# Kernel tuning notes

Measured on AMD Instinct MI355X. Metric: run time of the kernel, lower is better.

The kernel has to match this reference:

```python
import jax, jax.numpy as jnp
import numpy as np

L, D, H, G, HS, I, V, B, T = 4, 1024, 16, 4, 64, 2816, 32000, 4, 512
THETA = 10000.0
EPS = 1e-6


def setup_inputs() -> dict:
    key = jax.random.key(0)
    ks = jax.random.split(key, 10)
    s = 0.02
    return {
        "input_ids": jax.random.randint(ks[0], (B, T), 0, V),
        "embed": jax.random.normal(ks[1], (V, D)) * s,      # tied with lm_head
        "q_w": jax.random.normal(ks[2], (L, D, D)) * s,     # torch Linear: [out, in]
        "q_b": jax.random.normal(ks[3], (L, D)) * s,
        "kv_w": jax.random.normal(ks[4], (L, 2 * G * HS, D)) * s,
        "kv_b": jax.random.normal(ks[5], (L, 2 * G * HS)) * s,
        "o_w": jax.random.normal(ks[6], (L, D, D)) * s,
        "ln1_w": jnp.ones((L, D)),
        "ln2_w": jnp.ones((L, D)),
        "gate_w": jax.random.normal(ks[7], (L, I, D)) * s,
        "up_w": jax.random.normal(ks[8], (L, I, D)) * s,
        "down_w": jax.random.normal(ks[9], (L, D, I)) * s,
        "last_w": jnp.ones((D,)),
    }


def rms_norm(x, w):
    return x * jax.lax.rsqrt(jnp.mean(x * x, axis=-1, keepdims=True) + EPS) * w


def rope_tables(t, hs):
    inv_freq = 1.0 / (THETA ** (jnp.arange(0, hs, 2, dtype=jnp.float32) / hs))
    ang = jnp.arange(t, dtype=jnp.float32)[:, None] * inv_freq[None, :]  # [T, hs/2]
    emb = jnp.concatenate([ang, ang], axis=-1)                           # [T, hs]
    return jnp.cos(emb), jnp.sin(emb)


def rotate_half(x):
    x1, x2 = jnp.split(x, 2, axis=-1)
    return jnp.concatenate([-x2, x1], axis=-1)


def reference(input_ids, embed, q_w, q_b, kv_w, kv_b, o_w, ln1_w, ln2_w, gate_w, up_w, down_w, last_w):
    x = embed[input_ids]  # [B, T, D]
    cos, sin = rope_tables(T, HS)                    # [T, HS] (buffers, const)
    c, s_ = cos[None, None], sin[None, None]         # [1, 1, T, HS]
    causal = jnp.tril(jnp.ones((T, T), dtype=bool))
    scale = 1.0 / np.sqrt(HS).astype(np.float32)
    for l in range(L):
        h = rms_norm(x, ln1_w[l])
        q = (h @ q_w[l].T + q_b[l]).reshape(B, T, H, HS).transpose(0, 2, 1, 3)  # bhtd
        kv = h @ kv_w[l].T + kv_b[l]
        k, v = jnp.split(kv, 2, axis=-1)
        k = k.reshape(B, T, G, HS).transpose(0, 2, 1, 3)  # bgtd
        v = v.reshape(B, T, G, HS).transpose(0, 2, 1, 3)
        k = jnp.repeat(k, H // G, axis=1)  # GQA kv repeat -> bhtd
        v = jnp.repeat(v, H // G, axis=1)
        q = q * c + rotate_half(q) * s_
        k = k * c + rotate_half(k) * s_
        attn = jnp.einsum('bhtd,bhsd->bhts', q, k) * scale
        attn = jnp.where(causal, attn, -jnp.inf)
        attn = jax.nn.softmax(attn, axis=-1)
        o = jnp.einsum('bhts,bhsd->bhtd', attn, v).transpose(0, 2, 1, 3).reshape(B, T, D)
        x = x + o @ o_w[l].T  # o_proj has no bias
        h = rms_norm(x, ln2_w[l])
        x = x + (jax.nn.silu(h @ gate_w[l].T) * (h @ up_w[l].T)) @ down_w[l].T  # SwiGLU
    x = rms_norm(x, last_w)
    return x @ embed.T  # tied lm_head -> logits [B, T, V]
```

## Files before the change

kernel.cpp:

```cpp
#include <hip/hip_runtime.h>
#include <hip/hip_bf16.h>
#include <stdint.h>


typedef __bf16 bf16x8 __attribute__((ext_vector_type(8)));
typedef __bf16 bf16x4 __attribute__((ext_vector_type(4)));
typedef float  f32x4  __attribute__((ext_vector_type(4)));

#define AS1 __attribute__((address_space(1)))
#define AS3 __attribute__((address_space(3)))

__device__ __forceinline__ void gld_lds16(const void* g, void* l) {
  __builtin_amdgcn_global_load_lds((const AS1 void*)g, (AS3 void*)l, 16, 0, 0);
}

__global__ __launch_bounds__(256) void cvt_kernel(const float* __restrict__ in,
                                                  __bf16* __restrict__ out, int n4) {
  for (int i = blockIdx.x * 256 + threadIdx.x; i < n4; i += gridDim.x * 256) {
    f32x4 v = ((const f32x4*)in)[i];
    bf16x4 o;
#pragma unroll
    for (int j = 0; j < 4; ++j) o[j] = (__bf16)v[j];
    ((bf16x4*)out)[i] = o;
  }
}

__global__ __launch_bounds__(256) void embed_kernel(const int* __restrict__ ids,
                                                    const float* __restrict__ emb,
                                                    float* __restrict__ x) {
  const int tok = blockIdx.x;
  const float* src = emb + (size_t)ids[tok] * 1024;
  float* dst = x + (size_t)tok * 1024;
#pragma unroll
  for (int j = 0; j < 4; ++j) {
    const int d = threadIdx.x + j * 256;
    dst[d] = src[d];
  }
}

__global__ __launch_bounds__(256) void rmsnorm_kernel(const float* __restrict__ x,
                                                      const float* __restrict__ wgt,
                                                      __bf16* __restrict__ out) {
  const int row = blockIdx.x;
  const float* xr = x + (size_t)row * 1024;
  float v[4];
  float ss = 0.f;
#pragma unroll
  for (int j = 0; j < 4; ++j) { v[j] = xr[threadIdx.x + j * 256]; ss += v[j] * v[j]; }
#pragma unroll
  for (int m = 1; m < 64; m <<= 1) ss += __shfl_xor(ss, m, 64);
  __shared__ float red[4];
  if ((threadIdx.x & 63) == 0) red[threadIdx.x >> 6] = ss;
  __syncthreads();
  const float tot = red[0] + red[1] + red[2] + red[3];
  const float sc = rsqrtf(tot * (1.f / 1024.f) + 1e-6f);
#pragma unroll
  for (int j = 0; j < 4; ++j) {
    const int d = threadIdx.x + j * 256;
    out[(size_t)row * 1024 + d] = (__bf16)(v[j] * sc * wgt[d]);
  }
}

#define GEMM_PREAMBLE                                              \
  const int t = threadIdx.x;                                       \
  const int lane = t & 63;                                         \
  const int w = t >> 6, wr = w >> 1, wc = w & 1;                   \
  const int lr = lane & 15;                                        \
  const int lk = (lane >> 4) * 8;                                  \
  const int sr = t >> 2;                                           \
  const int scol = (t & 3) * 8;

#define FLAT_SWZ(BMC, BNC)                                         \
  const int chunk_ = (int)(gridDim.x >> 3);                        \
  const int wg_ = (blockIdx.x & 7) * chunk_ + (blockIdx.x >> 3);   \
  const int bm = wg_ % (BMC);                                      \
  const int rest_ = wg_ / (BMC);                                   \
  const int bn = rest_ % (BNC);                                    \
  const int ks = rest_ / (BNC);                                    \
  (void)ks;

#define GEMM_FRAGS_MFMA                                            \
  bf16x8 af[4], bfr[4];                                            \
  _Pragma("unroll") for (int m = 0; m < 4; ++m)                    \
    af[m] = *(const bf16x8*)&As[(wr * 64 + m * 16 + lr) * 32 + lk];\
  _Pragma("unroll") for (int n = 0; n < 4; ++n)                    \
    bfr[n] = *(const bf16x8*)&Bs[(wc * 64 + n * 16 + lr) * 32 + lk];\
  _Pragma("unroll") for (int m = 0; m < 4; ++m)                    \
    _Pragma("unroll") for (int n = 0; n < 4; ++n)                  \
      acc[m][n] = __builtin_amdgcn_mfma_f32_16x16x32_bf16(af[m], bfr[n], acc[m][n], 0, 0, 0);

template <int EPI, int BMC, int BNC, int KSP>
__global__ __launch_bounds__(256) void gemm_bt(const __bf16* __restrict__ A,
                                               const __bf16* __restrict__ Bb,
                                               float* __restrict__ Cf,
                                               int K, int ldc) {
  __shared__ __bf16 As[128 * 32];
  __shared__ __bf16 Bs[128 * 32];
  GEMM_PREAMBLE
  FLAT_SWZ(BMC, BNC)
  const int klen = K / KSP;
  const int kbeg = ks * klen;

  const __bf16* a0 = A + (size_t)(bm * 128 + sr) * K + scol;
  const __bf16* a1 = A + (size_t)(bm * 128 + 64 + sr) * K + scol;
  const __bf16* bb0 = Bb + (size_t)(bn * 128 + sr) * K + scol;
  const __bf16* bb1 = Bb + (size_t)(bn * 128 + 64 + sr) * K + scol;

  f32x4 acc[4][4] = {};
  for (int k0 = kbeg; k0 < kbeg + klen; k0 += 32) {
    gld_lds16(a0 + k0, &As[t * 8]);
    gld_lds16(a1 + k0, &As[2048 + t * 8]);
    gld_lds16(bb0 + k0, &Bs[t * 8]);
    gld_lds16(bb1 + k0, &Bs[2048 + t * 8]);
    __syncthreads();
    GEMM_FRAGS_MFMA
    __syncthreads();
  }
  const int r0 = bm * 128 + wr * 64 + (lane >> 4) * 4;
  const int c0 = bn * 128 + wc * 64 + lr;
#pragma unroll
  for (int m = 0; m < 4; ++m)
#pragma unroll
    for (int r = 0; r < 4; ++r) {
      const size_t rowoff = (size_t)(r0 + m * 16 + r) * ldc;
#pragma unroll
      for (int n = 0; n < 4; ++n) {
        if (EPI == 3) Cf[rowoff + c0 + n * 16] = acc[m][n][r];
        else          atomicAdd(&Cf[rowoff + c0 + n * 16], acc[m][n][r]);
      }
    }
}

__global__ __launch_bounds__(256) void qkv_gemm(const __bf16* __restrict__ A,
                                                const __bf16* __restrict__ qw,
                                                const __bf16* __restrict__ kvw,
                                                const float* __restrict__ q_b,
                                                const float* __restrict__ kv_b,
                                                __bf16* __restrict__ qb,
                                                __bf16* __restrict__ kvb) {
  const int K = 1024;
  __shared__ __bf16 As[128 * 32];
  __shared__ __bf16 Bs[128 * 32];
  GEMM_PREAMBLE
  FLAT_SWZ(16, 12)
  const bool isq = bn < 8;
  const int bnn = isq ? bn : bn - 8;
  const __bf16* Bw = (isq ? qw : kvw) + (size_t)(bnn * 128) * K;

  const __bf16* a0 = A + (size_t)(bm * 128 + sr) * K + scol;
  const __bf16* a1 = A + (size_t)(bm * 128 + 64 + sr) * K + scol;
  const __bf16* bb0 = Bw + (size_t)sr * K + scol;
  const __bf16* bb1 = Bw + (size_t)(64 + sr) * K + scol;

  f32x4 acc[4][4] = {};
  for (int k0 = 0; k0 < K; k0 += 32) {
    gld_lds16(a0 + k0, &As[t * 8]);
    gld_lds16(a1 + k0, &As[2048 + t * 8]);
    gld_lds16(bb0 + k0, &Bs[t * 8]);
    gld_lds16(bb1 + k0, &Bs[2048 + t * 8]);
    __syncthreads();
    GEMM_FRAGS_MFMA
    __syncthreads();
  }

  const int ldc = isq ? 1024 : 512;
  __bf16* out = isq ? qb : kvb;
  const float* bias = isq ? q_b : kv_b;
  const int cb = bnn * 128 + wc * 64;
  const bool dorope = isq || (cb < 256);
  float bv[4];
#pragma unroll
  for (int n = 0; n < 4; ++n) bv[n] = bias[cb + n * 16 + lr];
  float inv0 = __expf((float)lr * -0.28782313662425574f);
  float inv1 = __expf((float)(16 + lr) * -0.28782313662425574f);

  const int r0 = bm * 128 + wr * 64 + (lane >> 4) * 4;
#pragma unroll
  for (int m = 0; m < 4; ++m)
#pragma unroll
    for (int r = 0; r < 4; ++r) {
      const int row = r0 + m * 16 + r;
      float c4[4];
#pragma unroll
      for (int n = 0; n < 4; ++n) c4[n] = acc[m][n][r] + bv[n];
      if (dorope) {
        const float pos = (float)(row & 511);
        float sg, cg;
        __sincosf(pos * inv0, &sg, &cg);
        float x1 = c4[0], x2 = c4[2];
        c4[0] = x1 * cg - x2 * sg;
        c4[2] = x2 * cg + x1 * sg;
        __sincosf(pos * inv1, &sg, &cg);
        x1 = c4[1]; x2 = c4[3];
        c4[1] = x1 * cg - x2 * sg;
        c4[3] = x2 * cg + x1 * sg;
      }
      const size_t rowoff = (size_t)row * ldc;
#pragma unroll
      for (int n = 0; n < 4; ++n) out[rowoff + cb + n * 16 + lr] = (__bf16)c4[n];
    }
}

__global__ __launch_bounds__(256) void gateup_gemm(const __bf16* __restrict__ A,
                                                   const __bf16* __restrict__ gw,
                                                   const __bf16* __restrict__ uw,
                                                   __bf16* __restrict__ gbuf,
                                                   __bf16* __restrict__ ubuf) {
  const int K = 1024;
  __shared__ __bf16 As[128 * 32];
  __shared__ __bf16 Bs[128 * 32];
  GEMM_PREAMBLE
  FLAT_SWZ(16, 44)
  const bool isg = bn < 22;
  const int bnn = isg ? bn : bn - 22;
  const __bf16* Bw = (isg ? gw : uw) + (size_t)(bnn * 128) * K;
  __bf16* out = isg ? gbuf : ubuf;

  const __bf16* a0 = A + (size_t)(bm * 128 + sr) * K + scol;
  const __bf16* a1 = A + (size_t)(bm * 128 + 64 + sr) * K + scol;
  const __bf16* bb0 = Bw + (size_t)sr * K + scol;
  const __bf16* bb1 = Bw + (size_t)(64 + sr) * K + scol;

  f32x4 acc[4][4] = {};
  for (int k0 = 0; k0 < K; k0 += 32) {
    gld_lds16(a0 + k0, &As[t * 8]);
    gld_lds16(a1 + k0, &As[2048 + t * 8]);
    gld_lds16(bb0 + k0, &Bs[t * 8]);
    gld_lds16(bb1 + k0, &Bs[2048 + t * 8]);
    __syncthreads();
    GEMM_FRAGS_MFMA
    __syncthreads();
  }
  const int r0 = bm * 128 + wr * 64 + (lane >> 4) * 4;
  const int c0 = bnn * 128 + wc * 64 + lr;
#pragma unroll
  for (int m = 0; m < 4; ++m)
#pragma unroll
    for (int r = 0; r < 4; ++r) {
      const size_t rowoff = (size_t)(r0 + m * 16 + r) * 2816;
#pragma unroll
      for (int n = 0; n < 4; ++n) out[rowoff + c0 + n * 16] = (__bf16)acc[m][n][r];
    }
}

__global__ __launch_bounds__(256) void down_gemm(const __bf16* __restrict__ g,
                                                 const __bf16* __restrict__ u,
                                                 const __bf16* __restrict__ Bb,
                                                 float* __restrict__ Cf) {
  const int K = 2816;
  __shared__ __bf16 As[128 * 32];
  __shared__ __bf16 Bs[128 * 32];
  GEMM_PREAMBLE
  FLAT_SWZ(16, 8)
  const int klen = 1408;
  const int kbeg = ks * klen;

  const size_t arow0 = (size_t)(bm * 128 + sr) * K + scol;
  const size_t arow1 = (size_t)(bm * 128 + 64 + sr) * K + scol;
  const __bf16* bb0 = Bb + (size_t)(bn * 128 + sr) * K + scol;
  const __bf16* bb1 = Bb + (size_t)(bn * 128 + 64 + sr) * K + scol;

  f32x4 acc[4][4] = {};
  for (int k0 = kbeg; k0 < kbeg + klen; k0 += 32) {
    {
      bf16x8 gv0 = *(const bf16x8*)(g + arow0 + k0);
      bf16x8 uv0 = *(const bf16x8*)(u + arow0 + k0);
      bf16x8 gv1 = *(const bf16x8*)(g + arow1 + k0);
      bf16x8 uv1 = *(const bf16x8*)(u + arow1 + k0);
      bf16x8 s0, s1;
#pragma unroll
      for (int j = 0; j < 8; ++j) {
        const float gf = (float)gv0[j];
        s0[j] = (__bf16)(gf / (1.f + __expf(-gf)) * (float)uv0[j]);
      }
#pragma unroll
      for (int j = 0; j < 8; ++j) {
        const float gf = (float)gv1[j];
        s1[j] = (__bf16)(gf / (1.f + __expf(-gf)) * (float)uv1[j]);
      }
      *(bf16x8*)&As[t * 8] = s0;
      *(bf16x8*)&As[2048 + t * 8] = s1;
    }
    gld_lds16(bb0 + k0, &Bs[t * 8]);
    gld_lds16(bb1 + k0, &Bs[2048 + t * 8]);
    __syncthreads();
    GEMM_FRAGS_MFMA
    __syncthreads();
  }
  const int r0 = bm * 128 + wr * 64 + (lane >> 4) * 4;
  const int c0 = bn * 128 + wc * 64 + lr;
#pragma unroll
  for (int m = 0; m < 4; ++m)
#pragma unroll
    for (int r = 0; r < 4; ++r) {
      const size_t rowoff = (size_t)(r0 + m * 16 + r) * 1024;
#pragma unroll
      for (int n = 0; n < 4; ++n) atomicAdd(&Cf[rowoff + c0 + n * 16], acc[m][n][r]);
    }
}

__global__ __launch_bounds__(256) void attn_kernel(const __bf16* __restrict__ q,
                                                   const __bf16* __restrict__ kv,
                                                   __bf16* __restrict__ o) {
  const int qt = blockIdx.x, hh = blockIdx.y, b = blockIdx.z;
  const int g = hh >> 2;
  const int t = threadIdx.x, lane = t & 63, w = t >> 6;
  const int lr = lane & 15, lg = lane >> 4;

  __shared__ __bf16 Ks[64 * 64];
  __shared__ __bf16 Vt[64 * 72];
  __shared__ __bf16 Ps[64 * 72];

  bf16x8 qa[2];
  {
    const size_t qoff = ((size_t)(b * 512 + qt * 64 + w * 16 + lr)) * 1024 + hh * 64;
    qa[0] = *(const bf16x8*)(q + qoff + lg * 8);
    qa[1] = *(const bf16x8*)(q + qoff + 32 + lg * 8);
  }

  f32x4 acc_o[4] = {};
  float mrow[4], lrow[4];
#pragma unroll
  for (int r = 0; r < 4; ++r) { mrow[r] = -1e30f; lrow[r] = 0.f; }

  const int srow = t >> 3;
  const int sd = (((t & 7) ^ (srow & 7)) * 8);

  for (int kt = 0; kt <= qt; ++kt) {
    const size_t krow = ((size_t)(b * 512 + kt * 64 + srow)) * 512;
    gld_lds16(kv + krow + g * 64 + sd, &Ks[t * 8]);
    gld_lds16(kv + krow + 32 * 512 + g * 64 + sd, &Ks[2048 + t * 8]);
    {
      const __bf16* vsrc = kv + krow + 256 + g * 64 + sd;
      bf16x8 v0 = *(const bf16x8*)vsrc;
      bf16x8 v1 = *(const bf16x8*)(vsrc + 32 * 512);
#pragma unroll
      for (int j = 0; j < 8; ++j) Vt[(sd + j) * 72 + srow] = v0[j];
#pragma unroll
      for (int j = 0; j < 8; ++j) Vt[(sd + j) * 72 + srow + 32] = v1[j];
    }
    __syncthreads();

    f32x4 s[4] = {};
#pragma unroll
    for (int nf = 0; nf < 4; ++nf)
#pragma unroll
      for (int kc = 0; kc < 2; ++kc) {
        bf16x8 kb = *(const bf16x8*)&Ks[(nf * 16 + lr) * 64 + (((kc * 4 + lg) ^ (lr & 7)) * 8)];
        s[nf] = __builtin_amdgcn_mfma_f32_16x16x32_bf16(qa[kc], kb, s[nf], 0, 0, 0);
      }

    float pm[4][4], mx[4];
    const int qg = qt * 64 + w * 16 + lg * 4;
    const int kg = kt * 64 + lr;
#pragma unroll
    for (int r = 0; r < 4; ++r) mx[r] = -1e30f;
#pragma unroll
    for (int nf = 0; nf < 4; ++nf)
#pragma unroll
      for (int r = 0; r < 4; ++r) {
        float vv = s[nf][r] * 0.125f;
        vv = (kg + nf * 16 <= qg + r) ? vv : -1e30f;
        pm[nf][r] = vv;
        mx[r] = fmaxf(mx[r], vv);
      }
#pragma unroll
    for (int msk = 1; msk < 16; msk <<= 1)
#pragma unroll
      for (int r = 0; r < 4; ++r) mx[r] = fmaxf(mx[r], __shfl_xor(mx[r], msk, 64));

    float rs[4];
#pragma unroll
    for (int r = 0; r < 4; ++r) {
      const float mn = fmaxf(mrow[r], mx[r]);
      const float f = __expf(mrow[r] - mn);
      mrow[r] = mn;
      lrow[r] *= f;
#pragma unroll
      for (int df = 0; df < 4; ++df) acc_o[df][r] *= f;
      float rsum = 0.f;
#pragma unroll
      for (int nf = 0; nf < 4; ++nf) {
        const float pp = __expf(pm[nf][r] - mn);
        pm[nf][r] = pp;
        rsum += pp;
      }
      rs[r] = rsum;
    }
#pragma unroll
    for (int msk = 1; msk < 16; msk <<= 1)
#pragma unroll
      for (int r = 0; r < 4; ++r) rs[r] += __shfl_xor(rs[r], msk, 64);
#pragma unroll
    for (int r = 0; r < 4; ++r) lrow[r] += rs[r];

#pragma unroll
    for (int nf = 0; nf < 4; ++nf)
#pragma unroll
      for (int r = 0; r < 4; ++r)
        Ps[(w * 16 + lg * 4 + r) * 72 + nf * 16 + lr] = (__bf16)pm[nf][r];

#pragma unroll
    for (int df = 0; df < 4; ++df)
#pragma unroll
      for (int kc = 0; kc < 2; ++kc) {
        bf16x8 pa = *(const bf16x8*)&Ps[(w * 16 + lr) * 72 + kc * 32 + lg * 8];
        bf16x8 vb = *(const bf16x8*)&Vt[(df * 16 + lr) * 72 + kc * 32 + lg * 8];
        acc_o[df] = __builtin_amdgcn_mfma_f32_16x16x32_bf16(pa, vb, acc_o[df], 0, 0, 0);
      }
    __syncthreads();
  }

#pragma unroll
  for (int df = 0; df < 4; ++df)
#pragma unroll
    for (int r = 0; r < 4; ++r) {
      const int trow = qt * 64 + w * 16 + lg * 4 + r;
      o[((size_t)(b * 512 + trow)) * 1024 + hh * 64 + df * 16 + lr] =
          (__bf16)(acc_o[df][r] / lrow[r]);
    }
}

extern "C" void kernel_launch(void* const* d_in, const int* in_sizes, int n_in,
                              void* d_out, int out_size, void* d_ws, size_t ws_size,
                              hipStream_t stream) {
  const int* ids = (const int*)d_in[0];
  const float* emb_f = (const float*)d_in[1];
  const float* qw_f = (const float*)d_in[2];
  const float* q_b = (const float*)d_in[3];
  const float* kvw_f = (const float*)d_in[4];
  const float* kv_b = (const float*)d_in[5];
  const float* ow_f = (const float*)d_in[6];
  const float* ln1 = (const float*)d_in[7];
  const float* ln2 = (const float*)d_in[8];
  const float* gw_f = (const float*)d_in[9];
  const float* uw_f = (const float*)d_in[10];
  const float* dw_f = (const float*)d_in[11];
  const float* lw = (const float*)d_in[12];
  float* out = (float*)d_out;

  char* p = (char*)d_ws;
  float* x = (float*)p;        p += (size_t)2048 * 1024 * 4;
  __bf16* h = (__bf16*)p;      p += (size_t)2048 * 1024 * 2;
  __bf16* qb = (__bf16*)p;     p += (size_t)2048 * 1024 * 2;
  __bf16* kvb = (__bf16*)p;    p += (size_t)2048 * 512 * 2;
  __bf16* ao = (__bf16*)p;     p += (size_t)2048 * 1024 * 2;
  __bf16* gb = (__bf16*)p;     p += (size_t)2048 * 2816 * 2;
  __bf16* ub = (__bf16*)p;     p += (size_t)2048 * 2816 * 2;
  __bf16* emb_b = (__bf16*)p;  p += (size_t)32000 * 1024 * 2;
  __bf16* qw_b = (__bf16*)p;   p += (size_t)4 * 1024 * 1024 * 2;
  __bf16* kvw_b = (__bf16*)p;  p += (size_t)4 * 512 * 1024 * 2;
  __bf16* ow_b = (__bf16*)p;   p += (size_t)4 * 1024 * 1024 * 2;
  __bf16* gw_b = (__bf16*)p;   p += (size_t)4 * 2816 * 1024 * 2;
  __bf16* uw_b = (__bf16*)p;   p += (size_t)4 * 2816 * 1024 * 2;
  __bf16* dw_b = (__bf16*)p;   p += (size_t)4 * 2816 * 1024 * 2;

  cvt_kernel<<<2048, 256, 0, stream>>>(emb_f, emb_b, 32000 * 1024 / 4);
  cvt_kernel<<<1024, 256, 0, stream>>>(qw_f, qw_b, 4 * 1024 * 1024 / 4);
  cvt_kernel<<<1024, 256, 0, stream>>>(kvw_f, kvw_b, 4 * 512 * 1024 / 4);
  cvt_kernel<<<1024, 256, 0, stream>>>(ow_f, ow_b, 4 * 1024 * 1024 / 4);
  cvt_kernel<<<1024, 256, 0, stream>>>(gw_f, gw_b, 4 * 2816 * 1024 / 4);
  cvt_kernel<<<1024, 256, 0, stream>>>(uw_f, uw_b, 4 * 2816 * 1024 / 4);
  cvt_kernel<<<1024, 256, 0, stream>>>(dw_f, dw_b, 4 * 2816 * 1024 / 4);

  embed_kernel<<<2048, 256, 0, stream>>>(ids, emb_f, x);
  for (int l = 0; l < 4; ++l) {
    rmsnorm_kernel<<<2048, 256, 0, stream>>>(x, ln1 + l * 1024, h);
    qkv_gemm<<<192, 256, 0, stream>>>(
        h, qw_b + (size_t)l * 1024 * 1024, kvw_b + (size_t)l * 512 * 1024,
        q_b + l * 1024, kv_b + l * 512, qb, kvb);
    attn_kernel<<<dim3(8, 16, 4), 256, 0, stream>>>(qb, kvb, ao);
    gemm_bt<4, 16, 8, 2><<<256, 256, 0, stream>>>(
        ao, ow_b + (size_t)l * 1024 * 1024, x, 1024, 1024);
    rmsnorm_kernel<<<2048, 256, 0, stream>>>(x, ln2 + l * 1024, h);
    gateup_gemm<<<704, 256, 0, stream>>>(
        h, gw_b + (size_t)l * 2816 * 1024, uw_b + (size_t)l * 2816 * 1024, gb, ub);
    down_gemm<<<256, 256, 0, stream>>>(
        gb, ub, dw_b + (size_t)l * 1024 * 2816, x);
  }
  rmsnorm_kernel<<<2048, 256, 0, stream>>>(x, lw, h);
  gemm_bt<3, 16, 250, 1><<<4000, 256, 0, stream>>>(h, emb_b, out, 1024, 32000);
}
```

Baseline: 1.141 ms.

## Add dedicated 256x256 double-buffered LM-head GEMM and load K directly in attention

Replaces the generic gemm_bt used for the 2048x32000x1024 LM-head with a dedicated 512-thread kernel. It uses 256x256 tiles, double-buffered LDS staging via global_load_lds, XOR-swizzled LDS reads, a blockIdx remap for L2 locality, setprio around the MFMAs, and nontemporal output stores. The attention kernel drops its K shared-memory tile and has each lane load K fragments straight from global memory, and the fp32->bf16 conversion kernel switches to nontemporal loads. The large tiles and LDS footprint raise per-block resource use, and the direct K loads in attention read the same data redundantly across waves without LDS sharing.

```diff
diff --git a/kernel.cpp b/kernel.cpp
--- a/kernel.cpp
+++ b/kernel.cpp
@@ -17,7 +17,7 @@
 __global__ __launch_bounds__(256) void cvt_kernel(const float* __restrict__ in,
                                                   __bf16* __restrict__ out, int n4) {
   for (int i = blockIdx.x * 256 + threadIdx.x; i < n4; i += gridDim.x * 256) {
-    f32x4 v = ((const f32x4*)in)[i];
+    f32x4 v = __builtin_nontemporal_load(&((const f32x4*)in)[i]);
     bf16x4 o;
 #pragma unroll
     for (int j = 0; j < 4; ++j) o[j] = (__bf16)v[j];
@@ -299,6 +299,108 @@
     }
 }
 
+__global__ __launch_bounds__(512, 2) void lmhead_gemm(const __bf16* __restrict__ A,
+                                                      const __bf16* __restrict__ Bb,
+                                                      float* __restrict__ C) {
+  __shared__ __bf16 lds[2][4][8192];
+  const int t = threadIdx.x;
+  const int lane = t & 63;
+  const int w = t >> 6;
+  const int wr = w >> 2;
+  const int wc = w & 3;
+  const int lr = lane & 15;
+  const int lg = lane >> 4;
+  const int sx = (lr & 7) << 4;
+
+  const int wg = (blockIdx.x & 7) * 125 + (blockIdx.x >> 3);
+  const int bm = wg & 7;
+  const int bn = wg >> 3;
+
+  int srow[2], scol[2];
+#pragma unroll
+  for (int j = 0; j < 2; ++j) {
+    const int q = (t + j * 512) * 16;
+    const int row = q >> 7;
+    const int p = q ^ ((row & 7) << 4);
+    srow[j] = row;
+    scol[j] = (p & 127) >> 1;
+  }
+
+  auto STAGE = [&](int buf, int kt) {
+#pragma unroll
+    for (int ht = 0; ht < 4; ++ht) {
+      const __bf16* base = (ht < 2)
+          ? A + (size_t)(bm * 256 + ht * 128) * 1024
+          : Bb + (size_t)(bn * 256 + (ht - 2) * 128) * 1024;
+#pragma unroll
+      for (int j = 0; j < 2; ++j) {
+        gld_lds16(base + (size_t)srow[j] * 1024 + kt * 64 + scol[j],
+                  (char*)&lds[buf][ht][0] + (size_t)(t + j * 512) * 16);
+      }
+    }
+  };
+
+  STAGE(0, 0);
+  STAGE(1, 1);
+
+  f32x4 acc[8][4] = {};
+  for (int kt = 0; kt < 16; ++kt) {
+    const int cur = kt & 1;
+    if (kt < 15) asm volatile("s_waitcnt vmcnt(8)" ::: "memory");
+    else         asm volatile("s_waitcnt vmcnt(0)" ::: "memory");
+    __builtin_amdgcn_s_barrier();
+
+    const char* Ab = (const char*)&lds[cur][wr][0];
+    const char* Bbs = (const char*)&lds[cur][2 + (wc >> 1)][0];
+    const int rB0 = (wc & 1) * 64;
+#pragma unroll
+    for (int ph = 0; ph < 4; ++ph) {
+      const int m0 = (ph >> 1) * 4;
+      const int n0 = (ph & 1) * 2;
+      bf16x8 af[4][2], bfr[2][2];
+#pragma unroll
+      for (int mi = 0; mi < 4; ++mi)
+#pragma unroll
+        for (int ksl = 0; ksl < 2; ++ksl) {
+          const int row = (m0 + mi) * 16 + lr;
+          af[mi][ksl] = *(const bf16x8*)(Ab + ((row * 128 + ksl * 64 + lg * 16) ^ sx));
+        }
+#pragma unroll
+      for (int ni = 0; ni < 2; ++ni)
+#pragma unroll
+        for (int ksl = 0; ksl < 2; ++ksl) {
+          const int row = rB0 + (n0 + ni) * 16 + lr;
+          bfr[ni][ksl] = *(const bf16x8*)(Bbs + ((row * 128 + ksl * 64 + lg * 16) ^ sx));
+        }
+      __builtin_amdgcn_s_setprio(1);
+#pragma unroll
+      for (int mi = 0; mi < 4; ++mi)
+#pragma unroll
+        for (int ni = 0; ni < 2; ++ni)
+#pragma unroll
+          for (int ksl = 0; ksl < 2; ++ksl)
+            acc[m0 + mi][n0 + ni] = __builtin_amdgcn_mfma_f32_16x16x32_bf16(
+                af[mi][ksl], bfr[ni][ksl], acc[m0 + mi][n0 + ni], 0, 0, 0);
+      __builtin_amdgcn_s_setprio(0);
+    }
+    asm volatile("s_waitcnt lgkmcnt(0)" ::: "memory");
+    __builtin_amdgcn_s_barrier();
+    if (kt + 2 < 16) STAGE(cur, kt + 2);
+  }
+
+  const int r0 = bm * 256 + wr * 128 + lg * 4;
+  const int c0 = bn * 256 + wc * 64 + lr;
+#pragma unroll
+  for (int m = 0; m < 8; ++m)
+#pragma unroll
+    for (int r = 0; r < 4; ++r) {
+      float* crow = C + (size_t)(r0 + m * 16 + r) * 32000 + c0;
+#pragma unroll
+      for (int n = 0; n < 4; ++n)
+        __builtin_nontemporal_store(acc[m][n][r], crow + n * 16);
+    }
+}
+
 __global__ __launch_bounds__(256) void attn_kernel(const __bf16* __restrict__ q,
                                                    const __bf16* __restrict__ kv,
                                                    __bf16* __restrict__ o) {
@@ -307,7 +409,6 @@
   const int t = threadIdx.x, lane = t & 63, w = t >> 6;
   const int lr = lane & 15, lg = lane >> 4;
 
-  __shared__ __bf16 Ks[64 * 64];
   __shared__ __bf16 Vt[64 * 72];
   __shared__ __bf16 Ps[64 * 72];
 
@@ -324,31 +425,35 @@
   for (int r = 0; r < 4; ++r) { mrow[r] = -1e30f; lrow[r] = 0.f; }
 
   const int srow = t >> 3;
-  const int sd = (((t & 7) ^ (srow & 7)) * 8);
+  const int sdv = (t & 7) * 8;
 
   for (int kt = 0; kt <= qt; ++kt) {
     const size_t krow = ((size_t)(b * 512 + kt * 64 + srow)) * 512;
-    gld_lds16(kv + krow + g * 64 + sd, &Ks[t * 8]);
-    gld_lds16(kv + krow + 32 * 512 + g * 64 + sd, &Ks[2048 + t * 8]);
     {
-      const __bf16* vsrc = kv + krow + 256 + g * 64 + sd;
+      const __bf16* vsrc = kv + krow + 256 + g * 64 + sdv;
       bf16x8 v0 = *(const bf16x8*)vsrc;
       bf16x8 v1 = *(const bf16x8*)(vsrc + 32 * 512);
 #pragma unroll
-      for (int j = 0; j < 8; ++j) Vt[(sd + j) * 72 + srow] = v0[j];
-#pragma unroll
-      for (int j = 0; j < 8; ++j) Vt[(sd + j) * 72 + srow + 32] = v1[j];
-    }
-    __syncthreads();
+      for (int j = 0; j < 8; ++j) Vt[(sdv + j) * 72 + srow] = v0[j];
+#pragma unroll
+      for (int j = 0; j < 8; ++j) Vt[(sdv + j) * 72 + srow + 32] = v1[j];
+    }
+    __syncthreads();
+
+    bf16x8 kb[4][2];
+#pragma unroll
+    for (int nf = 0; nf < 4; ++nf)
+#pragma unroll
+      for (int kc = 0; kc < 2; ++kc)
+        kb[nf][kc] = *(const bf16x8*)(kv +
+            ((size_t)(b * 512 + kt * 64 + nf * 16 + lr)) * 512 + g * 64 + kc * 32 + lg * 8);
 
     f32x4 s[4] = {};
 #pragma unroll
     for (int nf = 0; nf < 4; ++nf)
 #pragma unroll
-      for (int kc = 0; kc < 2; ++kc) {
-        bf16x8 kb = *(const bf16x8*)&Ks[(nf * 16 + lr) * 64 + (((kc * 4 + lg) ^ (lr & 7)) * 8)];
-        s[nf] = __builtin_amdgcn_mfma_f32_16x16x32_bf16(qa[kc], kb, s[nf], 0, 0, 0);
-      }
+      for (int kc = 0; kc < 2; ++kc)
+        s[nf] = __builtin_amdgcn_mfma_f32_16x16x32_bf16(qa[kc], kb[nf][kc], s[nf], 0, 0, 0);
 
     float pm[4][4], mx[4];
     const int qg = qt * 64 + w * 16 + lg * 4;
@@ -479,5 +584,5 @@
         gb, ub, dw_b + (size_t)l * 1024 * 2816, x);
   }
   rmsnorm_kernel<<<2048, 256, 0, stream>>>(x, lw, h);
-  gemm_bt<3, 16, 250, 1><<<4000, 256, 0, stream>>>(h, emb_b, out, 1024, 32000);
-}
+  lmhead_gemm<<<1000, 512, 0, stream>>>(h, emb_b, out);
+}
```

Measured after the change: 1.064 ms. 6.7% less time.
